# Optimization experiments

Hardware: AMD Instinct MI355X
Metric: run time of the kernel (lower is better)

## Reference

```python
import jax, jax.numpy as jnp
import numpy as np

N_EMBD = 1024
H_DIM = 1024
NB = 16          # blocks resolved by _find_dynamic_num_blocks for all projections
N_MEM = 128
N_FORG = H_DIM - N_MEM
RANK = 64
LOG_DT_INIT = -2.0
EPS = 1.1920929e-07  # torch fp32 finfo eps used by F.rms_norm


def rms_norm(x):
    return x * jax.lax.rsqrt(jnp.mean(jnp.square(x), axis=-1, keepdims=True) + EPS)


def silu(x):
    return x * jax.nn.sigmoid(x)


def blockdiag(x, w):
    # x: [..., nb*bi], w: [nb, bo, bi] -> [..., nb*bo]
    nb, bo, bi = w.shape
    xs = x.reshape(*x.shape[:-1], nb, bi)
    y = jnp.einsum('...ni,noi->...no', xs, w)
    return y.reshape(*x.shape[:-1], nb * bo)


def causal_scan(drive, a):
    # drive: [B,T,D] float32, a: [D] per-channel decay; causal conv with kernel a^t via FFT
    B, T, D = drive.shape
    steps = jnp.arange(T, dtype=jnp.float32)
    kernel = jnp.exp(jnp.log(jnp.maximum(a, 1e-6))[:, None] * steps[None, :])  # [D,T]
    n_fft = 1 << int(2 * T - 1).bit_length()
    df = jnp.fft.rfft(drive.astype(jnp.float32).transpose(0, 2, 1), n=n_fft, axis=-1)
    kf = jnp.fft.rfft(kernel, n=n_fft, axis=-1)
    y = jnp.fft.irfft(df * kf[None], n=n_fft, axis=-1)[..., :T]
    return y.transpose(0, 2, 1).astype(drive.dtype)


def geom_gain(a, K):
    one_minus = 1.0 - a
    safe = jnp.maximum(one_minus, 1e-8)
    return jnp.where(jnp.abs(one_minus) < 1e-6,
                     jnp.full_like(a, float(K)),
                     (1.0 - a ** K) / safe)


def setup_inputs() -> dict:
    key = jax.random.key(0)
    ks = jax.random.split(key, 10)
    s = 0.02
    bi_e, bo_h = N_EMBD // NB, H_DIM // NB
    bi_p = (2 * N_EMBD + H_DIM) // NB
    bo_e = N_EMBD // NB
    return {
        'x': jax.random.normal(ks[0], (4, 4096, N_EMBD), dtype=jnp.float32),
        'active_k': 4,
        'b_seq_w': jax.random.normal(ks[1], (NB, bo_h, bi_e), jnp.float32) * s,
        'b_depth_w': jax.random.normal(ks[2], (NB, bo_h, bi_e), jnp.float32) * s,
        'w_post_w': jax.random.normal(ks[3], (NB, bo_h, bi_p), jnp.float32) * s,
        'w_local_w': jax.random.normal(ks[4], (NB, bo_e, H_DIM // NB), jnp.float32) * s,
        'lr_A': jax.random.normal(ks[5], (N_EMBD, RANK), jnp.float32) * s,
        'lr_B': jax.random.normal(ks[6], (RANK, H_DIM), jnp.float32) * s,
        'log_A_seq': jnp.zeros((H_DIM,), jnp.float32),
        'log_dt_seq': jnp.full((H_DIM,), LOG_DT_INIT, jnp.float32),
        'log_A_depth': jnp.zeros((N_FORG,), jnp.float32),
        'log_dt_depth': jnp.full((N_FORG,), LOG_DT_INIT, jnp.float32),
    }


def reference(x, active_k, b_seq_w, b_depth_w, w_post_w, w_local_w, lr_A, lr_B,
              log_A_seq, log_dt_seq, log_A_depth, log_dt_depth):
    K = int(active_k)
    e = rms_norm(x)
    shifted_e = jnp.pad(e[:, :-1], ((0, 0), (1, 0), (0, 0)))
    a_seq = jnp.exp(-jnp.exp(log_A_seq) * jnp.exp(log_dt_seq))
    h_seq = causal_scan(silu(blockdiag(e, b_seq_w)), a_seq)
    a_forg = jnp.exp(-jnp.exp(log_A_depth) * jnp.exp(log_dt_depth))
    a_depth = jnp.concatenate([jnp.ones((N_MEM,), a_forg.dtype), a_forg], axis=0)
    gain = geom_gain(a_depth, K).astype(x.dtype)
    h_depth = gain * silu(blockdiag(e, b_depth_w))
    h = h_seq + h_depth
    r = silu(blockdiag(jnp.concatenate([rms_norm(h), e, shifted_e], axis=-1), w_post_w))
    out = x + blockdiag(r, w_local_w) + (r @ lr_B.T) @ lr_A.T
    return out
```

## Files before the change

kernel.cpp:

```cpp
#include <hip/hip_runtime.h>

#define B_ 4
#define T_ 4096
#define D_ 1024
#define R_ (B_*T_)
#define CHUNK_ 64
#define NCH_ (T_/CHUNK_)
#define EPS_ 1.1920929e-07f

typedef unsigned short ushort_t;
typedef __attribute__((ext_vector_type(8))) short short8;
typedef __attribute__((ext_vector_type(4))) float f32x4;

__device__ __forceinline__ float silu_f(float v){ return v / (1.0f + __expf(-v)); }

__device__ __forceinline__ ushort_t f2bf(float f){
    unsigned u = __float_as_uint(f);
    unsigned r = u + 0x7fffu + ((u>>16)&1u);
    return (ushort_t)(r>>16);
}
__device__ __forceinline__ float bf2f(ushort_t s){ return __uint_as_float(((unsigned)s)<<16); }

__device__ __forceinline__ f32x4 mfma16(short8 a, short8 b, f32x4 c){
    return __builtin_amdgcn_mfma_f32_16x16x32_bf16(a, b, c, 0, 0, 0);
}

__global__ void prep_k(const float* __restrict__ s0, const float* __restrict__ s1,
                       const float* __restrict__ s2, const float* __restrict__ s3,
                       const float* __restrict__ s4, const float* __restrict__ s5,
                       ushort_t* __restrict__ d0, ushort_t* __restrict__ d1,
                       ushort_t* __restrict__ d2, ushort_t* __restrict__ d3,
                       ushort_t* __restrict__ d4, ushort_t* __restrict__ d5,
                       const float* __restrict__ logA_seq, const float* __restrict__ logdt_seq,
                       const float* __restrict__ logA_dep, const float* __restrict__ logdt_dep,
                       const int* __restrict__ active_k,
                       float* __restrict__ aseq, float* __restrict__ apowC, float* __restrict__ gain){
    int i = blockIdx.x*256 + threadIdx.x;
    if      (i < 65536)   d0[i] = f2bf(s0[i]);
    else if (i < 131072)  d1[i-65536] = f2bf(s1[i-65536]);
    else if (i < 327680)  d2[i-131072] = f2bf(s2[i-131072]);
    else if (i < 393216)  d3[i-327680] = f2bf(s3[i-327680]);
    else if (i < 458752)  d4[i-393216] = f2bf(s4[i-393216]);
    else if (i < 524288)  d5[i-458752] = f2bf(s5[i-458752]);
    else if (i < 524288 + D_){
        int d = i - 524288;
        float K = (float)(*active_k);
        float a = expf(-expf(logA_seq[d]) * expf(logdt_seq[d]));
        a = fmaxf(a, 1e-6f);
        aseq[d] = a;
        apowC[d] = powf(a, (float)CHUNK_);
        float g;
        if (d < 128) {
            g = K;
        } else {
            float ad = expf(-expf(logA_dep[d-128]) * expf(logdt_dep[d-128]));
            float om = 1.0f - ad;
            if (fabsf(om) < 1e-6f) g = K;
            else g = (1.0f - powf(ad, K)) / fmaxf(om, 1e-8f);
        }
        gain[d] = g;
    }
}

__global__ __launch_bounds__(256) void rmsbf_k(const float* __restrict__ x, ushort_t* __restrict__ e){
    int row = blockIdx.x;
    int tid = threadIdx.x;
    float4 v = ((const float4*)(x + (size_t)row*D_))[tid];
    float ss = v.x*v.x + v.y*v.y + v.z*v.z + v.w*v.w;
    for (int off=32; off; off>>=1) ss += __shfl_down(ss, off, 64);
    __shared__ float red[4];
    if ((tid&63)==0) red[tid>>6] = ss;
    __syncthreads();
    float tot = red[0]+red[1]+red[2]+red[3];
    float scale = 1.0f / sqrtf(tot*(1.0f/D_) + EPS_);
    ushort4 o;
    o.x = f2bf(v.x*scale); o.y = f2bf(v.y*scale); o.z = f2bf(v.z*scale); o.w = f2bf(v.w*scale);
    ((ushort4*)(e + (size_t)row*D_))[tid] = o;
}

__global__ __launch_bounds__(256) void bd2s_k(const ushort_t* __restrict__ e,
        const ushort_t* __restrict__ wseq, const ushort_t* __restrict__ wdep,
        const float* __restrict__ gain, const float* __restrict__ aseq,
        ushort_t* __restrict__ hloc, ushort_t* __restrict__ hdep, float* __restrict__ carry){
    __shared__ __align__(16) ushort_t sd[4][64][72];
    __shared__ __align__(16) ushort_t sh[4][16][72];
    int wave = threadIdx.x>>6, lane = threadIdx.x&63;
    int m = lane&15, quad = lane>>4;
    int orow = lane>>2, oq = lane&3;
    int n = blockIdx.y;
    int chunk0 = blockIdx.x*256 + wave*64;

    short8 bs[2][4], bd[2][4];
    #pragma unroll
    for (int s=0;s<2;++s)
        #pragma unroll
        for (int c=0;c<4;++c){
            bs[s][c] = *(const short8*)(wseq + n*4096 + (c*16+m)*64 + s*32 + quad*8);
            bd[s][c] = *(const short8*)(wdep + n*4096 + (c*16+m)*64 + s*32 + quad*8);
        }
    float g[4];
    #pragma unroll
    for (int c=0;c<4;++c) g[c] = gain[n*64 + c*16 + m];

    #pragma unroll
    for (int t=0;t<4;++t){
        int r0 = chunk0 + t*16;
        const ushort_t* ab = e + (size_t)(r0+m)*D_ + n*64 + quad*8;
        short8 a0 = *(const short8*)ab;
        short8 a1 = *(const short8*)(ab + 32);
        f32x4 accs[4], accd[4];
        #pragma unroll
        for (int c=0;c<4;++c){
            accs[c]=(f32x4)0.f; accd[c]=(f32x4)0.f;
            accs[c]=mfma16(a0, bs[0][c], accs[c]);
            accd[c]=mfma16(a0, bd[0][c], accd[c]);
            accs[c]=mfma16(a1, bs[1][c], accs[c]);
            accd[c]=mfma16(a1, bd[1][c], accd[c]);
        }
        #pragma unroll
        for (int c=0;c<4;++c)
            #pragma unroll
            for (int r=0;r<4;++r){
                sd[wave][t*16+quad*4+r][c*16+m] = f2bf(silu_f(accs[c][r]));
                sh[wave][quad*4+r][c*16+m]      = f2bf(g[c]*silu_f(accd[c][r]));
            }
        ushort_t* hb = hdep + (size_t)(r0+orow)*D_ + n*64;
        #pragma unroll
        for (int it=0;it<2;++it)
            *(short8*)(hb + (it*4+oq)*8) = *(const short8*)&sh[wave][orow][(it*4+oq)*8];
    }
    float a = aseq[n*64 + lane];
    float hh = 0.f;
    #pragma unroll 8
    for (int s=0;s<64;++s){
        hh = fmaf(a, hh, bf2f(sd[wave][s][lane]));
        sd[wave][s][lane] = f2bf(hh);
    }
    carry[(size_t)(chunk0>>6)*D_ + n*64 + lane] = hh;
    #pragma unroll
    for (int t=0;t<4;++t){
        ushort_t* db = hloc + (size_t)(chunk0 + t*16 + orow)*D_ + n*64;
        #pragma unroll
        for (int it=0;it<2;++it)
            *(short8*)(db + (it*4+oq)*8) = *(const short8*)&sd[wave][t*16+orow][(it*4+oq)*8];
    }
}

__global__ __launch_bounds__(256) void scan2_k(float* __restrict__ carry, const float* __restrict__ apowC){
    int tid = blockIdx.x*256 + threadIdx.x;
    int d = tid & (D_-1);
    int b = tid >> 10;
    float aC = apowC[d];
    float pref = 0.f;
    for (int c=0;c<NCH_;++c){
        size_t idx = (size_t)(b*NCH_+c)*D_ + d;
        float s = carry[idx];
        carry[idx] = pref;
        pref = fmaf(aC, pref, s);
    }
}

__global__ __launch_bounds__(256) void scan3_k(const ushort_t* __restrict__ hloc,
                                               const ushort_t* __restrict__ hdep,
                                               const float* __restrict__ aseq,
                                               const float* __restrict__ carry,
                                               ushort_t* __restrict__ h){
    int tid = blockIdx.x*256 + threadIdx.x;
    int d  = tid & (D_-1);
    int bc = tid >> 10;
    int c  = bc & (NCH_-1);
    int b  = bc >> 6;
    float a = aseq[d];
    float P = carry[(size_t)bc*D_ + d];
    size_t base = ((size_t)(b*T_ + c*CHUNK_))*D_ + d;
    float apow = a;
    #pragma unroll 4
    for (int s=0; s<CHUNK_; ++s){
        size_t idx = base + (size_t)s*D_;
        h[idx] = f2bf(bf2f(hloc[idx]) + P*apow + bf2f(hdep[idx]));
        apow *= a;
    }
}

__global__ __launch_bounds__(128) void hn_k(const ushort_t* __restrict__ h, ushort_t* __restrict__ hn){
    int row = blockIdx.x;
    int tid = threadIdx.x;
    short8 v = *(const short8*)(h + (size_t)row*D_ + tid*8);
    float f[8];
    float ss = 0.f;
    #pragma unroll
    for (int j=0;j<8;++j){ f[j] = bf2f((ushort_t)v[j]); ss += f[j]*f[j]; }
    for (int off=32; off; off>>=1) ss += __shfl_down(ss, off, 64);
    __shared__ float red[2];
    if ((tid&63)==0) red[tid>>6] = ss;
    __syncthreads();
    float scale = rsqrtf((red[0]+red[1])*(1.0f/D_) + EPS_);
    short8 o;
    #pragma unroll
    for (int j=0;j<8;++j) o[j] = (short)f2bf(f[j]*scale);
    *(short8*)(hn + (size_t)row*D_ + tid*8) = o;
}

__global__ __launch_bounds__(256) void post_k(const ushort_t* __restrict__ hn,
                                              const ushort_t* __restrict__ e,
                                              const ushort_t* __restrict__ wpost, ushort_t* __restrict__ rout){
    __shared__ __align__(16) ushort_t st[4][16][72];
    int wave = threadIdx.x>>6, lane = threadIdx.x&63;
    int m = lane&15, quad = lane>>4;
    int orow = lane>>2, oq = lane&3;
    int n = blockIdx.y;

    short8 bw[6][4];
    #pragma unroll
    for (int s=0;s<6;++s)
        #pragma unroll
        for (int c=0;c<4;++c)
            bw[s][c] = *(const short8*)(wpost + n*(64*192) + (c*16+m)*192 + s*32 + quad*8);

    #pragma unroll
    for (int t=0;t<4;++t){
        int r0 = blockIdx.x*256 + wave*64 + t*16;
        int row = r0 + m;
        bool zrow = ((row & (T_-1)) == 0);
        short8 af[6];
        #pragma unroll
        for (int s=0;s<6;++s){
            int g0 = n*192 + s*32;
            if (g0 < 1024){
                af[s] = *(const short8*)(hn + (size_t)row*D_ + g0 + quad*8);
            } else if (g0 < 2048){
                af[s] = *(const short8*)(e + (size_t)row*D_ + (g0-1024) + quad*8);
            } else {
                if (zrow) af[s] = short8{0,0,0,0,0,0,0,0};
                else      af[s] = *(const short8*)(e + (size_t)(row-1)*D_ + (g0-2048) + quad*8);
            }
        }
        f32x4 acc[4];
        #pragma unroll
        for (int c=0;c<4;++c) acc[c]=(f32x4)0.f;
        #pragma unroll
        for (int s=0;s<6;++s)
            #pragma unroll
            for (int c=0;c<4;++c)
                acc[c] = mfma16(af[s], bw[s][c], acc[c]);
        #pragma unroll
        for (int c=0;c<4;++c)
            #pragma unroll
            for (int r=0;r<4;++r)
                st[wave][quad*4+r][c*16+m] = f2bf(silu_f(acc[c][r]));
        ushort_t* db = rout + (size_t)(r0+orow)*D_ + n*64;
        #pragma unroll
        for (int it=0;it<2;++it)
            *(short8*)(db + (it*4+oq)*8) = *(const short8*)&st[wave][orow][(it*4+oq)*8];
    }
}

__global__ __launch_bounds__(256) void rlow_k(const ushort_t* __restrict__ r, const ushort_t* __restrict__ lrB,
                                              ushort_t* __restrict__ rlow){
    __shared__ __align__(16) ushort_t st[4][16][72];
    int wave = threadIdx.x>>6, lane = threadIdx.x&63;
    int m = lane&15, quad = lane>>4;
    int orow = lane>>2, oq = lane&3;
    int r0 = (blockIdx.x*4 + wave)*16;
    f32x4 acc[4];
    #pragma unroll
    for (int c=0;c<4;++c) acc[c]=(f32x4)0.f;
    const ushort_t* ab = r + (size_t)(r0+m)*D_ + quad*8;
    #pragma unroll 4
    for (int s=0;s<32;++s){
        short8 a = *(const short8*)(ab + s*32);
        #pragma unroll
        for (int c=0;c<4;++c){
            short8 b = *(const short8*)(lrB + (c*16+m)*1024 + s*32 + quad*8);
            acc[c] = mfma16(a, b, acc[c]);
        }
    }
    #pragma unroll
    for (int c=0;c<4;++c)
        #pragma unroll
        for (int r2=0;r2<4;++r2)
            st[wave][quad*4+r2][c*16+m] = f2bf(acc[c][r2]);
    ushort_t* db = rlow + (size_t)(r0+orow)*64;
    #pragma unroll
    for (int it=0;it<2;++it)
        *(short8*)(db + (it*4+oq)*8) = *(const short8*)&st[wave][orow][(it*4+oq)*8];
}

__global__ __launch_bounds__(256) void out_k(const float* __restrict__ x, const ushort_t* __restrict__ r,
        const ushort_t* __restrict__ rlow, const ushort_t* __restrict__ wloc, const ushort_t* __restrict__ lrA,
        float* __restrict__ out){
    __shared__ __align__(16) float st[4][16][68];
    int wave = threadIdx.x>>6, lane = threadIdx.x&63;
    int m = lane&15, quad = lane>>4;
    int orow = lane>>2, oq = lane&3;
    int n = blockIdx.y;

    short8 wl[2][4], la[4][2];
    #pragma unroll
    for (int c=0;c<4;++c)
        #pragma unroll
        for (int s=0;s<2;++s){
            wl[s][c] = *(const short8*)(wloc + n*4096 + (c*16+m)*64 + s*32 + quad*8);
            la[c][s] = *(const short8*)(lrA + (size_t)(n*64 + c*16 + m)*64 + s*32 + quad*8);
        }
    #pragma unroll
    for (int t=0;t<4;++t){
        int r0 = blockIdx.x*256 + wave*64 + t*16;
        const float* xb = x + (size_t)(r0+orow)*D_ + n*64;
        float4 xv[4];
        #pragma unroll
        for (int it=0;it<4;++it) xv[it] = *(const float4*)(xb + (it*4+oq)*4);

        const ushort_t* lb = rlow + (size_t)(r0+m)*64 + quad*8;
        short8 al0 = *(const short8*)lb;
        short8 al1 = *(const short8*)(lb + 32);
        const ushort_t* ab = r + (size_t)(r0+m)*D_ + n*64 + quad*8;
        short8 ar0 = *(const short8*)ab;
        short8 ar1 = *(const short8*)(ab + 32);
        f32x4 acc[4];
        #pragma unroll
        for (int c=0;c<4;++c){
            acc[c]=(f32x4)0.f;
            acc[c]=mfma16(al0, la[c][0], acc[c]);
            acc[c]=mfma16(al1, la[c][1], acc[c]);
            acc[c]=mfma16(ar0, wl[0][c], acc[c]);
            acc[c]=mfma16(ar1, wl[1][c], acc[c]);
        }
        #pragma unroll
        for (int c=0;c<4;++c)
            #pragma unroll
            for (int r2=0;r2<4;++r2)
                st[wave][quad*4+r2][c*16+m] = acc[c][r2];
        float* ob = out + (size_t)(r0+orow)*D_ + n*64;
        #pragma unroll
        for (int it=0;it<4;++it){
            float4 v = *(const float4*)&st[wave][orow][(it*4+oq)*4];
            v.x += xv[it].x; v.y += xv[it].y; v.z += xv[it].z; v.w += xv[it].w;
            *(float4*)(ob + (it*4+oq)*4) = v;
        }
    }
}

extern "C" void kernel_launch(void* const* d_in, const int* in_sizes, int n_in,
                              void* d_out, int out_size, void* d_ws, size_t ws_size,
                              hipStream_t stream) {
    const float* x         = (const float*)d_in[0];
    const int*   active_k  = (const int*)  d_in[1];
    const float* b_seq_w   = (const float*)d_in[2];
    const float* b_depth_w = (const float*)d_in[3];
    const float* w_post_w  = (const float*)d_in[4];
    const float* w_local_w = (const float*)d_in[5];
    const float* lr_A      = (const float*)d_in[6];
    const float* lr_B      = (const float*)d_in[7];
    const float* logA_seq  = (const float*)d_in[8];
    const float* logdt_seq = (const float*)d_in[9];
    const float* logA_dep  = (const float*)d_in[10];
    const float* logdt_dep = (const float*)d_in[11];

    float* ws    = (float*)d_ws;
    float* carry = ws;
    float* aseq  = carry + (size_t)B_*NCH_*D_;
    float* apowC = aseq + D_;
    float* gain  = apowC + D_;
    ushort_t* ub       = (ushort_t*)(gain + D_);
    ushort_t* e_bf     = ub;
    ushort_t* hloc_bf  = e_bf + (size_t)R_*D_;
    ushort_t* hdep_bf  = hloc_bf + (size_t)R_*D_;
    ushort_t* h_bf     = hdep_bf + (size_t)R_*D_;
    ushort_t* r_bf     = h_bf + (size_t)R_*D_;
    ushort_t* rlow_bf  = r_bf + (size_t)R_*D_;
    ushort_t* wseq_bf  = rlow_bf + (size_t)R_*64;
    ushort_t* wdep_bf  = wseq_bf + 65536;
    ushort_t* wpost_bf = wdep_bf + 65536;
    ushort_t* wloc_bf  = wpost_bf + 196608;
    ushort_t* lrA_bf   = wloc_bf + 65536;
    ushort_t* lrB_bf   = lrA_bf + 65536;
    ushort_t* hn_bf    = hloc_bf;

    prep_k<<<(524288 + D_ + 255)/256, 256, 0, stream>>>(
        b_seq_w, b_depth_w, w_post_w, w_local_w, lr_A, lr_B,
        wseq_bf, wdep_bf, wpost_bf, wloc_bf, lrA_bf, lrB_bf,
        logA_seq, logdt_seq, logA_dep, logdt_dep, active_k, aseq, apowC, gain);

    rmsbf_k<<<R_, 256, 0, stream>>>(x, e_bf);
    bd2s_k <<<dim3(R_/256, 16), 256, 0, stream>>>(e_bf, wseq_bf, wdep_bf, gain, aseq,
                                                  hloc_bf, hdep_bf, carry);
    scan2_k<<<(B_*D_)/256, 256, 0, stream>>>(carry, apowC);
    scan3_k<<<(B_*NCH_*D_)/256, 256, 0, stream>>>(hloc_bf, hdep_bf, aseq, carry, h_bf);
    hn_k   <<<R_, 128, 0, stream>>>(h_bf, hn_bf);
    post_k <<<dim3(R_/256, 16), 256, 0, stream>>>(hn_bf, e_bf, wpost_bf, r_bf);
    rlow_k <<<R_/64, 256, 0, stream>>>(r_bf, lrB_bf, rlow_bf);
    out_k  <<<dim3(R_/256, 16), 256, 0, stream>>>(x, r_bf, rlow_bf, wloc_bf, lrA_bf, (float*)d_out);
}
```

Before: 301.7 us.

## Split-K low-rank projection across waves and halve rows per block in post/out

The rlow kernel now has the four waves of a block split the K=1024 reduction for one 16-row tile, reducing the partial sums through shared memory in fp32 before the bf16 store. This gives four times as many blocks and shorter dependency chains per wave. post_k and out_k each process 128 rows per block instead of 256, which doubles the grid so more blocks can run concurrently, and out_k gets an occupancy launch bound. In exchange, each weight fragment loaded into registers is reused across fewer rows, and rlow adds a barrier plus shared-memory traffic.

New measurement: 346.1 us. +14.7%, slower.

```diff
diff --git a/kernel.cpp b/kernel.cpp
--- a/kernel.cpp
+++ b/kernel.cpp
@@ -218,8 +218,8 @@
             bw[s][c] = *(const short8*)(wpost + n*(64*192) + (c*16+m)*192 + s*32 + quad*8);
 
     #pragma unroll
-    for (int t=0;t<4;++t){
-        int r0 = blockIdx.x*256 + wave*64 + t*16;
+    for (int t=0;t<2;++t){
+        int r0 = blockIdx.x*128 + wave*32 + t*16;
         int row = r0 + m;
         bool zrow = ((row & (T_-1)) == 0);
         short8 af[6];
@@ -257,21 +257,20 @@
 
 __global__ __launch_bounds__(256) void rlow_k(const ushort_t* __restrict__ r, const ushort_t* __restrict__ lrB,
                                               ushort_t* __restrict__ rlow){
-    __shared__ __align__(16) ushort_t st[4][16][72];
+    __shared__ __align__(16) float sacc[4][16][68];
     int wave = threadIdx.x>>6, lane = threadIdx.x&63;
     int m = lane&15, quad = lane>>4;
-    int orow = lane>>2, oq = lane&3;
-    int r0 = (blockIdx.x*4 + wave)*16;
+    int r0 = blockIdx.x*16;
     f32x4 acc[4];
     #pragma unroll
     for (int c=0;c<4;++c) acc[c]=(f32x4)0.f;
-    const ushort_t* ab = r + (size_t)(r0+m)*D_ + quad*8;
-    #pragma unroll 4
-    for (int s=0;s<32;++s){
+    const ushort_t* ab = r + (size_t)(r0+m)*D_ + wave*256 + quad*8;
+    #pragma unroll
+    for (int s=0;s<8;++s){
         short8 a = *(const short8*)(ab + s*32);
         #pragma unroll
         for (int c=0;c<4;++c){
-            short8 b = *(const short8*)(lrB + (c*16+m)*1024 + s*32 + quad*8);
+            short8 b = *(const short8*)(lrB + (c*16+m)*1024 + wave*256 + s*32 + quad*8);
             acc[c] = mfma16(a, b, acc[c]);
         }
     }
@@ -279,14 +278,23 @@
     for (int c=0;c<4;++c)
         #pragma unroll
         for (int r2=0;r2<4;++r2)
-            st[wave][quad*4+r2][c*16+m] = f2bf(acc[c][r2]);
-    ushort_t* db = rlow + (size_t)(r0+orow)*64;
-    #pragma unroll
-    for (int it=0;it<2;++it)
-        *(short8*)(db + (it*4+oq)*8) = *(const short8*)&st[wave][orow][(it*4+oq)*8];
-}
-
-__global__ __launch_bounds__(256) void out_k(const float* __restrict__ x, const ushort_t* __restrict__ r,
+            sacc[wave][quad*4+r2][c*16+m] = acc[c][r2];
+    __syncthreads();
+    int row  = threadIdx.x>>4;
+    int col4 = (threadIdx.x&15)*4;
+    float4 v0 = *(const float4*)&sacc[0][row][col4];
+    float4 v1 = *(const float4*)&sacc[1][row][col4];
+    float4 v2 = *(const float4*)&sacc[2][row][col4];
+    float4 v3 = *(const float4*)&sacc[3][row][col4];
+    ushort4 o;
+    o.x = f2bf(v0.x+v1.x+v2.x+v3.x);
+    o.y = f2bf(v0.y+v1.y+v2.y+v3.y);
+    o.z = f2bf(v0.z+v1.z+v2.z+v3.z);
+    o.w = f2bf(v0.w+v1.w+v2.w+v3.w);
+    *(ushort4*)(rlow + (size_t)(r0+row)*64 + col4) = o;
+}
+
+__global__ __launch_bounds__(256, 8) void out_k(const float* __restrict__ x, const ushort_t* __restrict__ r,
         const ushort_t* __restrict__ rlow, const ushort_t* __restrict__ wloc, const ushort_t* __restrict__ lrA,
         float* __restrict__ out){
     __shared__ __align__(16) float st[4][16][68];
@@ -304,8 +312,8 @@
             la[c][s] = *(const short8*)(lrA + (size_t)(n*64 + c*16 + m)*64 + s*32 + quad*8);
         }
     #pragma unroll
-    for (int t=0;t<4;++t){
-        int r0 = blockIdx.x*256 + wave*64 + t*16;
+    for (int t=0;t<2;++t){
+        int r0 = blockIdx.x*128 + wave*32 + t*16;
         const float* xb = x + (size_t)(r0+orow)*D_ + n*64;
         float4 xv[4];
         #pragma unroll
@@ -388,7 +396,7 @@
     scan2_k<<<(B_*D_)/256, 256, 0, stream>>>(carry, apowC);
     scan3_k<<<(B_*NCH_*D_)/256, 256, 0, stream>>>(hloc_bf, hdep_bf, aseq, carry, h_bf);
     hn_k   <<<R_, 128, 0, stream>>>(h_bf, hn_bf);
-    post_k <<<dim3(R_/256, 16), 256, 0, stream>>>(hn_bf, e_bf, wpost_bf, r_bf);
-    rlow_k <<<R_/64, 256, 0, stream>>>(r_bf, lrB_bf, rlow_bf);
-    out_k  <<<dim3(R_/256, 16), 256, 0, stream>>>(x, r_bf, rlow_bf, wloc_bf, lrA_bf, (float*)d_out);
-}
+    post_k <<<dim3(R_/128, 16), 256, 0, stream>>>(hn_bf, e_bf, wpost_bf, r_bf);
+    rlow_k <<<R_/16, 256, 0, stream>>>(r_bf, lrB_bf, rlow_bf);
+    out_k  <<<dim3(R_/128, 16), 256, 0, stream>>>(x, r_bf, rlow_bf, wloc_bf, lrA_bf, (float*)d_out);
+}
```
